# Kernel optimization log

Measured on AMD Instinct MI355X. Metric: run time of the kernel, lower is better.

## Reference

```python
import jax, jax.numpy as jnp
import numpy as np

N = 4096
NEG_SLOPE = 0.2


def _gat_layer(x, src, dst, W, Wb, a, ab):
    # h = Linear(x); e_ij = a([h_i, h_j]) for each edge; dense softmax over dim=1; ELU
    h = x @ W + Wb                               # [N, D]
    D = h.shape[-1]
    e = h[src] @ a[:D] + h[dst] @ a[D:] + ab     # [E] per-edge attention logits
    n = x.shape[0]
    attn = jnp.full((n, n), -jnp.inf, dtype=x.dtype).at[src, dst].set(e)
    attn = jnp.where(attn > 0, attn, NEG_SLOPE * attn)   # leaky_relu (keeps -inf)
    attn = jax.nn.softmax(attn, axis=1)
    return jax.nn.elu(attn @ h)                  # sigma = ELU


def _multihead(x, src, dst, hW, hWb, ha, hab, oW, oWb, oa, oab):
    # concat=False: mean over head outputs, then out GATLayer
    heads = jax.vmap(lambda W, Wb, a, ab: _gat_layer(x, src, dst, W, Wb, a, ab))(hW, hWb, ha, hab)
    xm = heads.mean(axis=0)
    return _gat_layer(xm, src, dst, oW, oWb, oa, oab)


def setup_inputs() -> dict:
    key = jax.random.key(0)
    ks = jax.random.split(key, 20)
    in_dim, hid, out_dim, H, E = 512, 256, 128, 4, 131072
    x = jax.random.normal(ks[0], (N, in_dim), jnp.float32)
    edge_index = jax.random.randint(ks[1], (2, E), 0, N)
    # force self loops so every softmax row has at least one finite entry
    edge_index = edge_index.at[:, :N].set(jnp.broadcast_to(jnp.arange(N), (2, N)))

    def lin(k, shape, fan_in):
        return jax.random.uniform(k, shape, jnp.float32, -1.0, 1.0) / np.sqrt(fan_in).astype(np.float32)

    return {
        "x": x,
        "edge_index": edge_index,
        # layer 0 (MultiHeadGAT in_dim->hid)
        "l0_hW": lin(ks[2], (H, in_dim, hid), in_dim),
        "l0_hWb": lin(ks[3], (H, hid), in_dim),
        "l0_ha": lin(ks[4], (H, 2 * hid), 2 * hid),
        "l0_hab": lin(ks[5], (H,), 2 * hid),
        "l0_oW": lin(ks[6], (hid, hid), hid),
        "l0_oWb": lin(ks[7], (hid,), hid),
        "l0_oa": lin(ks[8], (2 * hid,), 2 * hid),
        "l0_oab": lin(ks[9], (), 2 * hid),
        # layer 1 (MultiHeadGAT hid->hid)
        "l1_hW": lin(ks[10], (H, hid, hid), hid),
        "l1_hWb": lin(ks[11], (H, hid), hid),
        "l1_ha": lin(ks[12], (H, 2 * hid), 2 * hid),
        "l1_hab": lin(ks[13], (H,), 2 * hid),
        "l1_oW": lin(ks[14], (hid, hid), hid),
        "l1_oWb": lin(ks[15], (hid,), hid),
        "l1_oa": lin(ks[16], (2 * hid,), 2 * hid),
        "l1_oab": lin(ks[17], (), 2 * hid),
        # final Linear(hid -> out_dim)
        "lin_W": lin(ks[18], (hid, out_dim), hid),
        "lin_b": lin(ks[19], (out_dim,), hid),
    }


def reference(x, edge_index, l0_hW, l0_hWb, l0_ha, l0_hab, l0_oW, l0_oWb, l0_oa, l0_oab,
              l1_hW, l1_hWb, l1_ha, l1_hab, l1_oW, l1_oWb, l1_oa, l1_oab, lin_W, lin_b):
    src, dst = edge_index[0], edge_index[1]
    lrelu = lambda v: jnp.where(v > 0, v, NEG_SLOPE * v)
    h = lrelu(_multihead(x, src, dst, l0_hW, l0_hWb, l0_ha, l0_hab, l0_oW, l0_oWb, l0_oa, l0_oab))
    h = lrelu(_multihead(h, src, dst, l1_hW, l1_hWb, l1_ha, l1_hab, l1_oW, l1_oWb, l1_oa, l1_oab))
    return h @ lin_W + lin_b  # [N, out_dim], flatten(1) is a no-op for 2D
```

## Files before the change

### kernel.cpp

```cpp
#include <hip/hip_runtime.h>
#include <hip/hip_bf16.h>
#include <math.h>

#define NEG_SLOPE 0.2f

constexpr int D = 256;
constexpr int HEADS = 4;
constexpr int MAXB = 128;

typedef __attribute__((ext_vector_type(8))) short short8;
typedef __attribute__((ext_vector_type(4))) float floatx4;

__device__ inline unsigned short bf16_hi_trunc(float v) {
  return (unsigned short)(__float_as_uint(v) >> 16);
}
__device__ inline float bf16_tof(unsigned short u) {
  return __uint_as_float(((unsigned int)u) << 16);
}
__device__ inline unsigned short bf16_rn(float v) {
  unsigned int b = __float_as_uint(v);
  b += 0x7fffu + ((b >> 16) & 1u);
  return (unsigned short)(b >> 16);
}
__device__ inline void split2(float v, unsigned short& hi, unsigned short& lo) {
  hi = bf16_hi_trunc(v);
  lo = bf16_rn(v - bf16_tof(hi));
}

__global__ void fill_kernel(const int* __restrict__ src, const int* __restrict__ dst,
                            int* __restrict__ cnt, int* __restrict__ colb, int E) {
  int k = blockIdx.x * blockDim.x + threadIdx.x;
  if (k < E) {
    int s = src[k];
    int pos = atomicAdd(&cnt[s], 1);
    if (pos < MAXB) colb[s * MAXB + pos] = dst[k];
  }
}

__global__ __launch_bounds__(128) void dedupe_kernel(const int* __restrict__ cnt,
                                                     int* __restrict__ colb, int Nn) {
  __shared__ int cs[MAXB];
  int i = blockIdx.x;
  int len = cnt[i];
  if (len > MAXB) len = MAXB;
  int tid = threadIdx.x;
  if (tid < len) cs[tid] = colb[i * MAXB + tid];
  __syncthreads();
  if (tid < len) {
    int c = cs[tid];
    bool dup = false;
    for (int s2 = 0; s2 < tid; ++s2)
      if (cs[s2] == c) { dup = true; break; }
    if (dup) colb[i * MAXB + tid] = -1;
  }
}

__global__ __launch_bounds__(256) void prep_kernel(
    int* __restrict__ zeroBase, int zeroN,
    const float* __restrict__ x, unsigned short* __restrict__ xhi, unsigned short* __restrict__ xlo,
    int xN4,
    const float* __restrict__ l0hW, unsigned short* __restrict__ l0hHi, unsigned short* __restrict__ l0hLo,
    const float* __restrict__ l1hW, unsigned short* __restrict__ l1hHi, unsigned short* __restrict__ l1hLo,
    const float* __restrict__ l0oW, unsigned short* __restrict__ l0oHi, unsigned short* __restrict__ l0oLo,
    const float* __restrict__ l1oW, unsigned short* __restrict__ l1oHi, unsigned short* __restrict__ l1oLo,
    const float* __restrict__ linW, unsigned short* __restrict__ linHi, unsigned short* __restrict__ linLo) {
  const int b = blockIdx.x;
  const int t = threadIdx.x;
  if (b < 528) {
    int idx = b * 256 + t;
    if (idx < zeroN) zeroBase[idx] = 0;
    return;
  }
  if (b < 2576) {
    int idx = (b - 528) * 256 + t;
    if (idx < xN4) {
      float4 v = ((const float4*)x)[idx];
      ushort4 h, l;
      split2(v.x, h.x, l.x);
      split2(v.y, h.y, l.y);
      split2(v.z, h.z, l.z);
      split2(v.w, h.w, l.w);
      ((ushort4*)xhi)[idx] = h;
      ((ushort4*)xlo)[idx] = l;
    }
    return;
  }
  __shared__ float tile[32][33];
  const int tr = t >> 5, tc = t & 31;
  if (b < 3088) {
    const int bi = b - 2576;
    const int kb = bi & 15;
    const int nb = (bi >> 4) & 7;
    const int h = bi >> 7;
    const int K = 512, N = 256;
    const int k0 = kb * 32, n0 = nb * 32;
    const float* B = l0hW + (size_t)h * K * N;
#pragma unroll
    for (int i = 0; i < 4; ++i)
      tile[tr + 8 * i][tc] = B[(size_t)(k0 + tr + 8 * i) * N + (n0 + tc)];
    __syncthreads();
    unsigned short* Thi = l0hHi + (size_t)h * N * K;
    unsigned short* Tlo = l0hLo + (size_t)h * N * K;
#pragma unroll
    for (int i = 0; i < 4; ++i) {
      int n = n0 + tr + 8 * i, k = k0 + tc;
      float v = tile[tc][tr + 8 * i];
      unsigned short hi, lo;
      split2(v, hi, lo);
      Thi[(size_t)n * K + k] = hi;
      Tlo[(size_t)n * K + k] = lo;
    }
    return;
  }
  const int bi = b - 3088;
  const int kb = bi & 7;
  const int nb = (bi >> 3) & 7;
  const int z = bi >> 6;
  const int K = 256;
  const int N = (z == 6) ? 128 : 256;
  const int k0 = kb * 32, n0 = nb * 32;
  if (n0 >= N) return;
  const float* B;
  unsigned short *Thi, *Tlo;
  if (z < 4) {
    B = l1hW + (size_t)z * K * 256;
    Thi = l1hHi + (size_t)z * 256 * K;
    Tlo = l1hLo + (size_t)z * 256 * K;
  } else if (z == 4) { B = l0oW; Thi = l0oHi; Tlo = l0oLo; }
  else if (z == 5)   { B = l1oW; Thi = l1oHi; Tlo = l1oLo; }
  else               { B = linW; Thi = linHi; Tlo = linLo; }
#pragma unroll
  for (int i = 0; i < 4; ++i)
    tile[tr + 8 * i][tc] = B[(size_t)(k0 + tr + 8 * i) * N + (n0 + tc)];
  __syncthreads();
#pragma unroll
  for (int i = 0; i < 4; ++i) {
    int n = n0 + tr + 8 * i, k = k0 + tc;
    float v = tile[tc][tr + 8 * i];
    unsigned short hi, lo;
    split2(v, hi, lo);
    Thi[(size_t)n * K + k] = hi;
    Tlo[(size_t)n * K + k] = lo;
  }
}

__global__ __launch_bounds__(256) void gemm_mfma_split(
    const unsigned short* __restrict__ Ahi, const unsigned short* __restrict__ Alo,
    const unsigned short* __restrict__ Bthi, const unsigned short* __restrict__ Btlo,
    const float* __restrict__ bias, float* __restrict__ C, unsigned short* __restrict__ Cb,
    const float* __restrict__ aptr, float* __restrict__ alphaB, float* __restrict__ betaB,
    int M, int N, int K) {
  constexpr int LSTR = 72;
  __shared__ unsigned short sA[2][64 * LSTR];
  __shared__ unsigned short sB[2][64 * LSTR];
  const int tid = threadIdx.x;
  const int bm = blockIdx.x * 64;
  const int gn = blockIdx.y * 64;
  const int head = (gn) / N;
  const int bn = gn - head * N;
  const int Htot = (int)((gridDim.y * 64) / N);

  const int lane = tid & 63;
  const int wv = tid >> 6;
  const int wm = (wv & 1) * 32;
  const int wn = (wv >> 1) * 32;
  const int q = lane >> 4;
  const int l15 = lane & 15;

  floatx4 acc[2][2];
#pragma unroll
  for (int i = 0; i < 2; ++i)
#pragma unroll
    for (int j = 0; j < 2; ++j) acc[i][j] = (floatx4)0.0f;

  for (int k0 = 0; k0 < K; k0 += 64) {
    short8 ra[2][2], rb[2][2];
#pragma unroll
    for (int i = 0; i < 2; ++i) {
      const int c = tid + 256 * i;
      const int row = c >> 3, koff = (c & 7) << 3;
      const size_t boff = (size_t)(gn + row) * K + k0 + koff;
      rb[0][i] = *(const short8*)(Bthi + boff);
      rb[1][i] = *(const short8*)(Btlo + boff);
      const size_t aoff = (size_t)(bm + row) * K + k0 + koff;
      ra[0][i] = *(const short8*)(Ahi + aoff);
      ra[1][i] = *(const short8*)(Alo + aoff);
    }
    __syncthreads();
#pragma unroll
    for (int i = 0; i < 2; ++i) {
      const int c = tid + 256 * i;
      const int row = c >> 3, koff = (c & 7) << 3;
      *(short8*)(&sA[0][row * LSTR + koff]) = ra[0][i];
      *(short8*)(&sA[1][row * LSTR + koff]) = ra[1][i];
      *(short8*)(&sB[0][row * LSTR + koff]) = rb[0][i];
      *(short8*)(&sB[1][row * LSTR + koff]) = rb[1][i];
    }
    __syncthreads();
#pragma unroll
    for (int kc = 0; kc < 2; ++kc) {
      const int ko = kc * 32 + q * 8;
      short8 aH[2], aL[2], bH[2], bL[2];
#pragma unroll
      for (int i = 0; i < 2; ++i) {
        aH[i] = *(const short8*)(&sA[0][(wm + i * 16 + l15) * LSTR + ko]);
        aL[i] = *(const short8*)(&sA[1][(wm + i * 16 + l15) * LSTR + ko]);
        bH[i] = *(const short8*)(&sB[0][(wn + i * 16 + l15) * LSTR + ko]);
        bL[i] = *(const short8*)(&sB[1][(wn + i * 16 + l15) * LSTR + ko]);
      }
#pragma unroll
      for (int i = 0; i < 2; ++i)
#pragma unroll
        for (int j = 0; j < 2; ++j) {
          acc[i][j] = __builtin_amdgcn_mfma_f32_16x16x32_bf16(aH[i], bH[j], acc[i][j], 0, 0, 0);
          acc[i][j] = __builtin_amdgcn_mfma_f32_16x16x32_bf16(aH[i], bL[j], acc[i][j], 0, 0, 0);
          acc[i][j] = __builtin_amdgcn_mfma_f32_16x16x32_bf16(aL[i], bH[j], acc[i][j], 0, 0, 0);
        }
    }
  }
  const size_t rowStride = (size_t)Htot * N;
  const size_t headOff = (size_t)head * N;
  const int colh0 = bn + wn + l15;
  const int colh1 = colh0 + 16;
  const float bv0 = bias[head * N + colh0];
  const float bv1 = bias[head * N + colh1];
  float as0 = 0.f, as1 = 0.f, ad0 = 0.f, ad1 = 0.f;
  if (aptr) {
    as0 = aptr[head * 2 * N + colh0];
    as1 = aptr[head * 2 * N + colh1];
    ad0 = aptr[head * 2 * N + N + colh0];
    ad1 = aptr[head * 2 * N + N + colh1];
  }
#pragma unroll
  for (int i = 0; i < 2; ++i) {
    const int rowb = bm + wm + i * 16 + q * 4;
#pragma unroll
    for (int r = 0; r < 4; ++r) {
      const float o0 = acc[i][0][r] + bv0;
      const float o1 = acc[i][1][r] + bv1;
      if (Cb) {
        Cb[(size_t)(rowb + r) * rowStride + headOff + colh0] = bf16_rn(o0);
        Cb[(size_t)(rowb + r) * rowStride + headOff + colh1] = bf16_rn(o1);
      } else {
        C[(size_t)(rowb + r) * N + colh0] = o0;
        C[(size_t)(rowb + r) * N + colh1] = o1;
      }
      if (aptr) {
        float pa = o0 * as0 + o1 * as1;
        float pb = o0 * ad0 + o1 * ad1;
#pragma unroll
        for (int off = 1; off < 16; off <<= 1) {
          pa += __shfl_xor(pa, off, 64);
          pb += __shfl_xor(pb, off, 64);
        }
        if (l15 == 0) {
          atomicAdd(&alphaB[(size_t)(rowb + r) * Htot + head], pa);
          atomicAdd(&betaB[(size_t)(rowb + r) * Htot + head], pb);
        }
      }
    }
  }
}

__global__ __launch_bounds__(256) void gemm_bias(
    const float* __restrict__ A, const float* __restrict__ B,
    const float* __restrict__ bias, float* __restrict__ C,
    int M, int N, int K) {
  __shared__ float As[16][68];
  __shared__ float Bs[16][68];
  const int tid = threadIdx.x;
  const int bm = blockIdx.x * 64;
  const int gn = blockIdx.y * 64;
  const int head = gn / N;
  const int bn = gn - head * N;
  const float* Bh = B + (size_t)head * K * N;

  const int tx = tid & 15;
  const int ty = tid >> 4;
  const int am = tid >> 2;
  const int ak = (tid & 3) << 2;
  const int bk = tid >> 4;
  const int bn4 = (tid & 15) << 2;

  float acc[4][4] = {};

  for (int k0 = 0; k0 < K; k0 += 16) {
    float4 av = *(const float4*)(A + (size_t)(bm + am) * K + (k0 + ak));
    float4 bv = *(const float4*)(Bh + (size_t)(k0 + bk) * N + (bn + bn4));
    __syncthreads();
    As[ak + 0][am] = av.x;
    As[ak + 1][am] = av.y;
    As[ak + 2][am] = av.z;
    As[ak + 3][am] = av.w;
    *(float4*)(&Bs[bk][bn4]) = bv;
    __syncthreads();
#pragma unroll
    for (int k = 0; k < 16; ++k) {
      float4 aa = *(const float4*)(&As[k][ty << 2]);
      float4 bb = *(const float4*)(&Bs[k][tx << 2]);
      acc[0][0] += aa.x * bb.x; acc[0][1] += aa.x * bb.y; acc[0][2] += aa.x * bb.z; acc[0][3] += aa.x * bb.w;
      acc[1][0] += aa.y * bb.x; acc[1][1] += aa.y * bb.y; acc[1][2] += aa.y * bb.z; acc[1][3] += aa.y * bb.w;
      acc[2][0] += aa.z * bb.x; acc[2][1] += aa.z * bb.y; acc[2][2] += aa.z * bb.z; acc[2][3] += aa.z * bb.w;
      acc[3][0] += aa.w * bb.x; acc[3][1] += aa.w * bb.y; acc[3][2] += aa.w * bb.z; acc[3][3] += aa.w * bb.w;
    }
  }
  float* Ch = C + (size_t)head * M * N;
  const float* bh = bias + (size_t)head * N;
  const int ccol = bn + (tx << 2);
  float4 bias4 = *(const float4*)(bh + ccol);
#pragma unroll
  for (int r = 0; r < 4; ++r) {
    int row = bm + (ty << 2) + r;
    float4 o;
    o.x = acc[r][0] + bias4.x;
    o.y = acc[r][1] + bias4.y;
    o.z = acc[r][2] + bias4.z;
    o.w = acc[r][3] + bias4.w;
    *(float4*)(Ch + (size_t)row * N + ccol) = o;
  }
}

__global__ __launch_bounds__(256) void alphabeta_kernel(
    const float* __restrict__ h, const float* __restrict__ a,
    float* __restrict__ alpha, float* __restrict__ beta, int Nn) {
  __shared__ float reda[4], redb[4];
  const int i = blockIdx.x;
  const int hh = blockIdx.y;
  const int tid = threadIdx.x;
  const int lane = tid & 63, wid = tid >> 6;
  float v = h[((size_t)hh * Nn + i) * D + tid];
  float pa = v * a[hh * 2 * D + tid];
  float pb = v * a[hh * 2 * D + D + tid];
#pragma unroll
  for (int off = 32; off > 0; off >>= 1) {
    pa += __shfl_xor(pa, off, 64);
    pb += __shfl_xor(pb, off, 64);
  }
  if (lane == 0) { reda[wid] = pa; redb[wid] = pb; }
  __syncthreads();
  if (tid == 0) {
    alpha[hh * Nn + i] = reda[0] + reda[1] + reda[2] + reda[3];
    beta[hh * Nn + i] = redb[0] + redb[1] + redb[2] + redb[3];
  }
}

__global__ __launch_bounds__(256) void attn4(
    const unsigned short* __restrict__ hB,
    const float* __restrict__ alpha, const float* __restrict__ beta,
    const float* __restrict__ ab, const int* __restrict__ cnt,
    const int* __restrict__ colb,
    unsigned short* __restrict__ oHi, unsigned short* __restrict__ oLo, int Nn) {
  const int tid = threadIdx.x;
  const int lane = tid & 63;
  const int wv = tid >> 6;
  const int i = blockIdx.x * 4 + wv;

  const unsigned short* hL = hB + (lane << 2);
  const float ai0 = alpha[i * HEADS + 0] + ab[0];
  const float ai1 = alpha[i * HEADS + 1] + ab[1];
  const float ai2 = alpha[i * HEADS + 2] + ab[2];
  const float ai3 = alpha[i * HEADS + 3] + ab[3];
  const int start = i * MAXB;
  int len = cnt[i];
  if (len > MAXB) len = MAXB;

  float m0 = -3.0e38f, m1 = -3.0e38f, m2 = -3.0e38f, m3 = -3.0e38f;
  float s0 = 0.f, s1 = 0.f, s2 = 0.f, s3 = 0.f;
  float4 A0 = make_float4(0.f, 0.f, 0.f, 0.f);
  float4 A1 = make_float4(0.f, 0.f, 0.f, 0.f);
  float4 A2 = make_float4(0.f, 0.f, 0.f, 0.f);
  float4 A3 = make_float4(0.f, 0.f, 0.f, 0.f);

  for (int t0 = 0; t0 < len; t0 += 64) {
    const int t = t0 + lane;
    const int c = (t < len) ? colb[start + t] : -1;
    float e0 = -3.0e38f, e1 = -3.0e38f, e2 = -3.0e38f, e3 = -3.0e38f;
    if (c >= 0) {
      const float4 b4 = *(const float4*)(beta + (size_t)c * HEADS);
      e0 = ai0 + b4.x; e1 = ai1 + b4.y; e2 = ai2 + b4.z; e3 = ai3 + b4.w;
      e0 = e0 > 0.0f ? e0 : NEG_SLOPE * e0;
      e1 = e1 > 0.0f ? e1 : NEG_SLOPE * e1;
      e2 = e2 > 0.0f ? e2 : NEG_SLOPE * e2;
      e3 = e3 > 0.0f ? e3 : NEG_SLOPE * e3;
    }
    float c0 = e0, c1 = e1, c2 = e2, c3 = e3;
#pragma unroll
    for (int off = 32; off > 0; off >>= 1) {
      c0 = fmaxf(c0, __shfl_xor(c0, off, 64));
      c1 = fmaxf(c1, __shfl_xor(c1, off, 64));
      c2 = fmaxf(c2, __shfl_xor(c2, off, 64));
      c3 = fmaxf(c3, __shfl_xor(c3, off, 64));
    }
    const float n0 = fmaxf(m0, c0), n1 = fmaxf(m1, c1);
    const float n2 = fmaxf(m2, c2), n3 = fmaxf(m3, c3);
    const float sc0 = __expf(m0 - n0), sc1 = __expf(m1 - n1);
    const float sc2 = __expf(m2 - n2), sc3 = __expf(m3 - n3);
    float w0 = 0.f, w1 = 0.f, w2 = 0.f, w3 = 0.f;
    if (c >= 0) {
      w0 = __expf(e0 - n0); w1 = __expf(e1 - n1);
      w2 = __expf(e2 - n2); w3 = __expf(e3 - n3);
    }
    float q0 = w0, q1 = w1, q2 = w2, q3 = w3;
#pragma unroll
    for (int off = 32; off > 0; off >>= 1) {
      q0 += __shfl_xor(q0, off, 64);
      q1 += __shfl_xor(q1, off, 64);
      q2 += __shfl_xor(q2, off, 64);
      q3 += __shfl_xor(q3, off, 64);
    }
    s0 = s0 * sc0 + q0; s1 = s1 * sc1 + q1;
    s2 = s2 * sc2 + q2; s3 = s3 * sc3 + q3;
    A0.x *= sc0; A0.y *= sc0; A0.z *= sc0; A0.w *= sc0;
    A1.x *= sc1; A1.y *= sc1; A1.z *= sc1; A1.w *= sc1;
    A2.x *= sc2; A2.y *= sc2; A2.z *= sc2; A2.w *= sc2;
    A3.x *= sc3; A3.y *= sc3; A3.z *= sc3; A3.w *= sc3;
    m0 = n0; m1 = n1; m2 = n2; m3 = n3;

    const int cS = (c >= 0) ? c : 0;
    const int cnt2 = min(64, len - t0);
    int j = 0;
    for (; j + 2 <= cnt2; j += 2) {
      const int ca = __shfl(cS, j);
      const int cb = __shfl(cS, j + 1);
      const float wa0 = __shfl(w0, j),     wa1 = __shfl(w1, j);
      const float wa2 = __shfl(w2, j),     wa3 = __shfl(w3, j);
      const float wb0 = __shfl(w0, j + 1), wb1 = __shfl(w1, j + 1);
      const float wb2 = __shfl(w2, j + 1), wb3 = __shfl(w3, j + 1);
      const unsigned short* pa = hL + (size_t)ca * (HEADS * D);
      const unsigned short* pb = hL + (size_t)cb * (HEADS * D);
      const ushort4 ua0 = *(const ushort4*)(pa);
      const ushort4 ua1 = *(const ushort4*)(pa + D);
      const ushort4 ua2 = *(const ushort4*)(pa + 2 * D);
      const ushort4 ua3 = *(const ushort4*)(pa + 3 * D);
      const ushort4 ub0 = *(const ushort4*)(pb);
      const ushort4 ub1 = *(const ushort4*)(pb + D);
      const ushort4 ub2 = *(const ushort4*)(pb + 2 * D);
      const ushort4 ub3 = *(const ushort4*)(pb + 3 * D);
      A0.x += wa0 * bf16_tof(ua0.x); A0.y += wa0 * bf16_tof(ua0.y);
      A0.z += wa0 * bf16_tof(ua0.z); A0.w += wa0 * bf16_tof(ua0.w);
      A1.x += wa1 * bf16_tof(ua1.x); A1.y += wa1 * bf16_tof(ua1.y);
      A1.z += wa1 * bf16_tof(ua1.z); A1.w += wa1 * bf16_tof(ua1.w);
      A2.x += wa2 * bf16_tof(ua2.x); A2.y += wa2 * bf16_tof(ua2.y);
      A2.z += wa2 * bf16_tof(ua2.z); A2.w += wa2 * bf16_tof(ua2.w);
      A3.x += wa3 * bf16_tof(ua3.x); A3.y += wa3 * bf16_tof(ua3.y);
      A3.z += wa3 * bf16_tof(ua3.z); A3.w += wa3 * bf16_tof(ua3.w);
      A0.x += wb0 * bf16_tof(ub0.x); A0.y += wb0 * bf16_tof(ub0.y);
      A0.z += wb0 * bf16_tof(ub0.z); A0.w += wb0 * bf16_tof(ub0.w);
      A1.x += wb1 * bf16_tof(ub1.x); A1.y += wb1 * bf16_tof(ub1.y);
      A1.z += wb1 * bf16_tof(ub1.z); A1.w += wb1 * bf16_tof(ub1.w);
      A2.x += wb2 * bf16_tof(ub2.x); A2.y += wb2 * bf16_tof(ub2.y);
      A2.z += wb2 * bf16_tof(ub2.z); A2.w += wb2 * bf16_tof(ub2.w);
      A3.x += wb3 * bf16_tof(ub3.x); A3.y += wb3 * bf16_tof(ub3.y);
      A3.z += wb3 * bf16_tof(ub3.z); A3.w += wb3 * bf16_tof(ub3.w);
    }
    for (; j < cnt2; ++j) {
      const int ca = __shfl(cS, j);
      const float wa0 = __shfl(w0, j), wa1 = __shfl(w1, j);
      const float wa2 = __shfl(w2, j), wa3 = __shfl(w3, j);
      const unsigned short* pa = hL + (size_t)ca * (HEADS * D);
      const ushort4 ua0 = *(const ushort4*)(pa);
      const ushort4 ua1 = *(const ushort4*)(pa + D);
      const ushort4 ua2 = *(const ushort4*)(pa + 2 * D);
      const ushort4 ua3 = *(const ushort4*)(pa + 3 * D);
      A0.x += wa0 * bf16_tof(ua0.x); A0.y += wa0 * bf16_tof(ua0.y);
      A0.z += wa0 * bf16_tof(ua0.z); A0.w += wa0 * bf16_tof(ua0.w);
      A1.x += wa1 * bf16_tof(ua1.x); A1.y += wa1 * bf16_tof(ua1.y);
      A1.z += wa1 * bf16_tof(ua1.z); A1.w += wa1 * bf16_tof(ua1.w);
      A2.x += wa2 * bf16_tof(ua2.x); A2.y += wa2 * bf16_tof(ua2.y);
      A2.z += wa2 * bf16_tof(ua2.z); A2.w += wa2 * bf16_tof(ua2.w);
      A3.x += wa3 * bf16_tof(ua3.x); A3.y += wa3 * bf16_tof(ua3.y);
      A3.z += wa3 * bf16_tof(ua3.z); A3.w += wa3 * bf16_tof(ua3.w);
    }
  }

  const float i0 = 1.0f / s0, i1 = 1.0f / s1, i2 = 1.0f / s2, i3 = 1.0f / s3;
  auto elu = [](float x) { return x > 0.0f ? x : expm1f(x); };
  float4 xm;
  xm.x = 0.25f * (elu(A0.x * i0) + elu(A1.x * i1) + elu(A2.x * i2) + elu(A3.x * i3));
  xm.y = 0.25f * (elu(A0.y * i0) + elu(A1.y * i1) + elu(A2.y * i2) + elu(A3.y * i3));
  xm.z = 0.25f * (elu(A0.z * i0) + elu(A1.z * i1) + elu(A2.z * i2) + elu(A3.z * i3));
  xm.w = 0.25f * (elu(A0.w * i0) + elu(A1.w * i1) + elu(A2.w * i2) + elu(A3.w * i3));
  ushort4 h4, l4;
  split2(xm.x, h4.x, l4.x);
  split2(xm.y, h4.y, l4.y);
  split2(xm.z, h4.z, l4.z);
  split2(xm.w, h4.w, l4.w);
  const size_t q4 = ((size_t)i * D >> 2) + lane;
  ((ushort4*)oHi)[q4] = h4;
  ((ushort4*)oLo)[q4] = l4;
}

template <int BF16H>
__global__ __launch_bounds__(256) void attn2(
    const float* __restrict__ h, const unsigned short* __restrict__ hB,
    const float* __restrict__ alpha, const float* __restrict__ beta,
    const float* __restrict__ ab, const int* __restrict__ cnt,
    const int* __restrict__ colb, float* __restrict__ out,
    unsigned short* __restrict__ oHi, unsigned short* __restrict__ oLo,
    int Nn, int H, int mode) {
  const int tid = threadIdx.x;
  const int lane = tid & 63;
  const int wv = tid >> 6;
  const int bx = blockIdx.x;
  const int head = bx % H;
  const int rowblk = bx / H;
  const int i = rowblk * 4 + wv;

  const float* hL = BF16H ? nullptr : (h + (size_t)head * Nn * D + (lane << 2));
  const unsigned short* hLB = BF16H ? (hB + (size_t)head * Nn * D + (lane << 2)) : nullptr;
  const float* betaH = beta + (size_t)head * Nn;
  const float ai = alpha[head * Nn + i] + ab[head];
  const int start = i * MAXB;
  int len = cnt[i];
  if (len > MAXB) len = MAXB;

  float m = -3.0e38f, s = 0.0f;
  float4 acc0 = make_float4(0.0f, 0.0f, 0.0f, 0.0f);
  float4 acc1 = make_float4(0.0f, 0.0f, 0.0f, 0.0f);

  for (int t0 = 0; t0 < len; t0 += 64) {
    const int t = t0 + lane;
    const int c = (t < len) ? colb[start + t] : -1;
    float e = -3.0e38f;
    if (c >= 0) {
      e = ai + betaH[c];
      e = e > 0.0f ? e : NEG_SLOPE * e;
    }
    float cm = e;
#pragma unroll
    for (int off = 32; off > 0; off >>= 1) cm = fmaxf(cm, __shfl_xor(cm, off, 64));
    const float newm = fmaxf(m, cm);
    const float scale = __expf(m - newm);
    const float w = (c >= 0) ? __expf(e - newm) : 0.0f;
    float cs = w;
#pragma unroll
    for (int off = 32; off > 0; off >>= 1) cs += __shfl_xor(cs, off, 64);
    s = s * scale + cs;
    acc0.x *= scale; acc0.y *= scale; acc0.z *= scale; acc0.w *= scale;
    acc1.x *= scale; acc1.y *= scale; acc1.z *= scale; acc1.w *= scale;
    m = newm;

    const int cS = (c >= 0) ? c : 0;
    const int cnt2 = min(64, len - t0);
    int j = 0;
    if constexpr (BF16H) {
      for (; j + 4 <= cnt2; j += 4) {
        const int c0 = __shfl(cS, j);     const float w0 = __shfl(w, j);
        const int c1 = __shfl(cS, j + 1); const float w1 = __shfl(w, j + 1);
        const int c2 = __shfl(cS, j + 2); const float w2 = __shfl(w, j + 2);
        const int c3 = __shfl(cS, j + 3); const float w3 = __shfl(w, j + 3);
        const ushort4 u0 = *(const ushort4*)(hLB + (size_t)c0 * D);
        const ushort4 u1 = *(const ushort4*)(hLB + (size_t)c1 * D);
        const ushort4 u2 = *(const ushort4*)(hLB + (size_t)c2 * D);
        const ushort4 u3 = *(const ushort4*)(hLB + (size_t)c3 * D);
        acc0.x += w0 * bf16_tof(u0.x); acc0.y += w0 * bf16_tof(u0.y);
        acc0.z += w0 * bf16_tof(u0.z); acc0.w += w0 * bf16_tof(u0.w);
        acc1.x += w1 * bf16_tof(u1.x); acc1.y += w1 * bf16_tof(u1.y);
        acc1.z += w1 * bf16_tof(u1.z); acc1.w += w1 * bf16_tof(u1.w);
        acc0.x += w2 * bf16_tof(u2.x); acc0.y += w2 * bf16_tof(u2.y);
        acc0.z += w2 * bf16_tof(u2.z); acc0.w += w2 * bf16_tof(u2.w);
        acc1.x += w3 * bf16_tof(u3.x); acc1.y += w3 * bf16_tof(u3.y);
        acc1.z += w3 * bf16_tof(u3.z); acc1.w += w3 * bf16_tof(u3.w);
      }
      for (; j < cnt2; ++j) {
        const int cj = __shfl(cS, j);
        const float wj = __shfl(w, j);
        const ushort4 u = *(const ushort4*)(hLB + (size_t)cj * D);
        acc0.x += wj * bf16_tof(u.x); acc0.y += wj * bf16_tof(u.y);
        acc0.z += wj * bf16_tof(u.z); acc0.w += wj * bf16_tof(u.w);
      }
    } else {
      for (; j + 4 <= cnt2; j += 4) {
        const int c0 = __shfl(cS, j);     const float w0 = __shfl(w, j);
        const int c1 = __shfl(cS, j + 1); const float w1 = __shfl(w, j + 1);
        const int c2 = __shfl(cS, j + 2); const float w2 = __shfl(w, j + 2);
        const int c3 = __shfl(cS, j + 3); const float w3 = __shfl(w, j + 3);
        const float4 h0 = *(const float4*)(hL + (size_t)c0 * D);
        const float4 h1 = *(const float4*)(hL + (size_t)c1 * D);
        const float4 h2 = *(const float4*)(hL + (size_t)c2 * D);
        const float4 h3 = *(const float4*)(hL + (size_t)c3 * D);
        acc0.x += w0 * h0.x; acc0.y += w0 * h0.y; acc0.z += w0 * h0.z; acc0.w += w0 * h0.w;
        acc1.x += w1 * h1.x; acc1.y += w1 * h1.y; acc1.z += w1 * h1.z; acc1.w += w1 * h1.w;
        acc0.x += w2 * h2.x; acc0.y += w2 * h2.y; acc0.z += w2 * h2.z; acc0.w += w2 * h2.w;
        acc1.x += w3 * h3.x; acc1.y += w3 * h3.y; acc1.z += w3 * h3.z; acc1.w += w3 * h3.w;
      }
      for (; j < cnt2; ++j) {
        const int cj = __shfl(cS, j);
        const float wj = __shfl(w, j);
        const float4 hv = *(const float4*)(hL + (size_t)cj * D);
        acc0.x += wj * hv.x; acc0.y += wj * hv.y;
        acc0.z += wj * hv.z; acc0.w += wj * hv.w;
      }
    }
  }

  const float inv = 1.0f / s;
  float4 v;
  v.x = (acc0.x + acc1.x) * inv; v.y = (acc0.y + acc1.y) * inv;
  v.z = (acc0.z + acc1.z) * inv; v.w = (acc0.w + acc1.w) * inv;
  v.x = v.x > 0.0f ? v.x : expm1f(v.x);
  v.y = v.y > 0.0f ? v.y : expm1f(v.y);
  v.z = v.z > 0.0f ? v.z : expm1f(v.z);
  v.w = v.w > 0.0f ? v.w : expm1f(v.w);

  if (mode == 1 || mode == 3) {
    v.x = v.x > 0.0f ? v.x : NEG_SLOPE * v.x;
    v.y = v.y > 0.0f ? v.y : NEG_SLOPE * v.y;
    v.z = v.z > 0.0f ? v.z : NEG_SLOPE * v.z;
    v.w = v.w > 0.0f ? v.w : NEG_SLOPE * v.w;
    if (mode == 1) {
      *(float4*)(out + (size_t)i * D + (lane << 2)) = v;
    } else {
      ushort4 h4, l4;
      split2(v.x, h4.x, l4.x);
      split2(v.y, h4.y, l4.y);
      split2(v.z, h4.z, l4.z);
      split2(v.w, h4.w, l4.w);
      const size_t q4 = ((size_t)i * D >> 2) + lane;
      ((ushort4*)oHi)[q4] = h4;
      ((ushort4*)oLo)[q4] = l4;
    }
  } else if (mode == 0) {
    if constexpr (BF16H) {
      ushort4 h4;
      h4.x = bf16_rn(v.x);
      h4.y = bf16_rn(v.y);
      h4.z = bf16_rn(v.z);
      h4.w = bf16_rn(v.w);
      const size_t q4 = (((size_t)head * Nn + i) * D >> 2) + lane;
      ((ushort4*)oHi)[q4] = h4;
    } else {
      *(float4*)(out + ((size_t)head * Nn + i) * D + (lane << 2)) = v;
    }
  } else {
    const float invH = 1.0f / (float)H;
    float* o = out + (size_t)i * D + (lane << 2);
    atomicAdd(o + 0, invH * v.x);
    atomicAdd(o + 1, invH * v.y);
    atomicAdd(o + 2, invH * v.z);
    atomicAdd(o + 3, invH * v.w);
  }
}

__global__ __launch_bounds__(256) void mean4_kernel(
    float* __restrict__ hsep, int total4) {
  int idx = blockIdx.x * blockDim.x + threadIdx.x;
  if (idx < total4) {
    float4* p = (float4*)hsep;
    float4 a = p[idx], b = p[idx + total4], c = p[idx + 2 * total4], d = p[idx + 3 * total4];
    float4 o;
    o.x = 0.25f * (a.x + b.x + c.x + d.x);
    o.y = 0.25f * (a.y + b.y + c.y + d.y);
    o.z = 0.25f * (a.z + b.z + c.z + d.z);
    o.w = 0.25f * (a.w + b.w + c.w + d.w);
    p[idx] = o;
  }
}

__global__ void zero_ints(int* __restrict__ p, int n) {
  int i = blockIdx.x * blockDim.x + threadIdx.x;
  if (i < n) p[i] = 0;
}

__global__ void zero_floats(float* __restrict__ p, int n) {
  int i = blockIdx.x * blockDim.x + threadIdx.x;
  if (i < n) p[i] = 0.0f;
}

extern "C" void kernel_launch(void* const* d_in, const int* in_sizes, int n_in,
                              void* d_out, int out_size, void* d_ws, size_t ws_size,
                              hipStream_t stream) {
  const float* x = (const float*)d_in[0];
  const int* eidx = (const int*)d_in[1];
  const float* l0_hW = (const float*)d_in[2];
  const float* l0_hWb = (const float*)d_in[3];
  const float* l0_ha = (const float*)d_in[4];
  const float* l0_hab = (const float*)d_in[5];
  const float* l0_oW = (const float*)d_in[6];
  const float* l0_oWb = (const float*)d_in[7];
  const float* l0_oa = (const float*)d_in[8];
  const float* l0_oab = (const float*)d_in[9];
  const float* l1_hW = (const float*)d_in[10];
  const float* l1_hWb = (const float*)d_in[11];
  const float* l1_ha = (const float*)d_in[12];
  const float* l1_hab = (const float*)d_in[13];
  const float* l1_oW = (const float*)d_in[14];
  const float* l1_oWb = (const float*)d_in[15];
  const float* l1_oa = (const float*)d_in[16];
  const float* l1_oab = (const float*)d_in[17];
  const float* lin_W = (const float*)d_in[18];
  const float* lin_b = (const float*)d_in[19];

  const int in_dim = 512;
  const int Nn = in_sizes[0] / in_dim;
  const int E = in_sizes[1] / 2;
  const int out_dim = 128;

  char* wsp = (char*)d_ws;
  auto alloc = [&](size_t bytes) {
    char* p = wsp;
    wsp += (bytes + 255) & ~(size_t)255;
    return p;
  };
  const size_t ndBytes = sizeof(float) * (size_t)Nn * D;
  const size_t mfmaNeed = 52000000;
  const bool mfma = ws_size >= mfmaNeed;

  if (mfma) {
    unsigned short* hbufB = (unsigned short*)alloc((size_t)HEADS * Nn * D * 2);
    unsigned short* houtB = (unsigned short*)alloc((size_t)Nn * D * 2);
    unsigned short* xmHi  = (unsigned short*)alloc((size_t)Nn * D * 2);
    unsigned short* xmLo  = (unsigned short*)alloc((size_t)Nn * D * 2);
    unsigned short* xhi  = (unsigned short*)alloc((size_t)Nn * in_dim * 2);
    unsigned short* xlo  = (unsigned short*)alloc((size_t)Nn * in_dim * 2);
    unsigned short* x1hi = xhi;
    unsigned short* x1lo = xlo;
    unsigned short* l0hHi = (unsigned short*)alloc((size_t)HEADS * in_dim * D * 2);
    unsigned short* l0hLo = (unsigned short*)alloc((size_t)HEADS * in_dim * D * 2);
    unsigned short* l1hHi = (unsigned short*)alloc((size_t)HEADS * D * D * 2);
    unsigned short* l1hLo = (unsigned short*)alloc((size_t)HEADS * D * D * 2);
    unsigned short* l0oHi = (unsigned short*)alloc((size_t)D * D * 2);
    unsigned short* l0oLo = (unsigned short*)alloc((size_t)D * D * 2);
    unsigned short* l1oHi = (unsigned short*)alloc((size_t)D * D * 2);
    unsigned short* l1oLo = (unsigned short*)alloc((size_t)D * D * 2);
    unsigned short* linHi = (unsigned short*)alloc((size_t)D * out_dim * 2);
    unsigned short* linLo = (unsigned short*)alloc((size_t)D * out_dim * 2);
    int* cnt     = (int*)alloc(sizeof(int) * Nn);
    float* abz   = (float*)alloc(sizeof(float) * 4 * 2 * HEADS * (size_t)Nn);
    int* colb    = (int*)alloc(sizeof(int) * (size_t)Nn * MAXB);
    auto alphaS = [&](int s) { return abz + (size_t)s * 2 * HEADS * Nn; };
    auto betaS  = [&](int s) { return abz + (size_t)s * 2 * HEADS * Nn + HEADS * Nn; };

    const int* src = eidx;
    const int* dst = eidx + E;

    const int zeroN = Nn + 4 * 2 * HEADS * Nn;
    prep_kernel<<<3536, 256, 0, stream>>>(
        cnt, zeroN,
        x, xhi, xlo, Nn * in_dim / 4,
        l0_hW, l0hHi, l0hLo, l1_hW, l1hHi, l1hLo,
        l0_oW, l0oHi, l0oLo, l1_oW, l1oHi, l1oLo, lin_W, linHi, linLo);

    fill_kernel<<<(E + 255) / 256, 256, 0, stream>>>(src, dst, cnt, colb, E);
    dedupe_kernel<<<Nn, 128, 0, stream>>>(cnt, colb, Nn);

    gemm_mfma_split<<<dim3(Nn / 64, HEADS * D / 64), 256, 0, stream>>>(
        xhi, xlo, l0hHi, l0hLo, l0_hWb, nullptr, hbufB,
        l0_ha, alphaS(0), betaS(0), Nn, D, in_dim);
    attn4<<<Nn / 4, 256, 0, stream>>>(hbufB, alphaS(0), betaS(0), l0_hab,
                                      cnt, colb, xmHi, xmLo, Nn);
    gemm_mfma_split<<<dim3(Nn / 64, D / 64), 256, 0, stream>>>(
        xmHi, xmLo, l0oHi, l0oLo, l0_oWb, nullptr, houtB,
        l0_oa, alphaS(1), betaS(1), Nn, D, D);
    attn2<1><<<Nn / 4, 256, 0, stream>>>(nullptr, houtB, alphaS(1), betaS(1), l0_oab,
                                         cnt, colb, nullptr, x1hi, x1lo, Nn, 1, 3);

    gemm_mfma_split<<<dim3(Nn / 64, HEADS * D / 64), 256, 0, stream>>>(
        x1hi, x1lo, l1hHi, l1hLo, l1_hWb, nullptr, hbufB,
        l1_ha, alphaS(2), betaS(2), Nn, D, D);
    attn4<<<Nn / 4, 256, 0, stream>>>(hbufB, alphaS(2), betaS(2), l1_hab,
                                      cnt, colb, xmHi, xmLo, Nn);
    gemm_mfma_split<<<dim3(Nn / 64, D / 64), 256, 0, stream>>>(
        xmHi, xmLo, l1oHi, l1oLo, l1_oWb, nullptr, houtB,
        l1_oa, alphaS(3), betaS(3), Nn, D, D);
    attn2<1><<<Nn / 4, 256, 0, stream>>>(nullptr, houtB, alphaS(3), betaS(3), l1_oab,
                                         cnt, colb, nullptr, x1hi, x1lo, Nn, 1, 3);

    gemm_mfma_split<<<dim3(Nn / 64, out_dim / 64), 256, 0, stream>>>(
        x1hi, x1lo, linHi, linLo, lin_b, (float*)d_out, nullptr,
        nullptr, nullptr, nullptr, Nn, out_dim, D);
    return;
  }

  const size_t smallBytes = sizeof(float) * 2 * HEADS * (size_t)Nn + sizeof(int) * (Nn + (size_t)Nn * MAXB) + 4096;
  const bool staged = ws_size >= (8 * ndBytes + 2 * ndBytes + smallBytes + 65536);

  float* hbuf  = (float*)alloc(ndBytes * HEADS);
  float* hsep  = staged ? (float*)alloc(ndBytes * HEADS) : nullptr;
  float* xm    = staged ? hsep : (float*)alloc(ndBytes);
  float* x1    = (float*)alloc(ndBytes);
  float* hout  = (float*)alloc(ndBytes);
  float* alpha = (float*)alloc(sizeof(float) * HEADS * (size_t)Nn);
  float* beta  = (float*)alloc(sizeof(float) * HEADS * (size_t)Nn);
  int* cnt     = (int*)alloc(sizeof(int) * Nn);
  int* colb    = (int*)alloc(sizeof(int) * (size_t)Nn * MAXB);

  const int* src = eidx;
  const int* dst = eidx + E;

  zero_ints<<<(Nn + 255) / 256, 256, 0, stream>>>(cnt, Nn);
  fill_kernel<<<(E + 255) / 256, 256, 0, stream>>>(src, dst, cnt, colb, E);
  dedupe_kernel<<<Nn, 128, 0, stream>>>(cnt, colb, Nn);

  const int total4 = Nn * D / 4;
  const int meanBlocks = (total4 + 255) / 256;

  gemm_bias<<<dim3(Nn / 64, HEADS * D / 64), 256, 0, stream>>>(x, l0_hW, l0_hWb, hbuf, Nn, D, in_dim);
  alphabeta_kernel<<<dim3(Nn, HEADS), 256, 0, stream>>>(hbuf, l0_ha, alpha, beta, Nn);
  if (staged) {
    attn2<0><<<HEADS * (Nn / 4), 256, 0, stream>>>(hbuf, nullptr, alpha, beta, l0_hab, cnt, colb, hsep, nullptr, nullptr, Nn, HEADS, 0);
    mean4_kernel<<<meanBlocks, 256, 0, stream>>>(hsep, total4);
  } else {
    zero_floats<<<(Nn * D + 255) / 256, 256, 0, stream>>>(xm, Nn * D);
    attn2<0><<<HEADS * (Nn / 4), 256, 0, stream>>>(hbuf, nullptr, alpha, beta, l0_hab, cnt, colb, xm, nullptr, nullptr, Nn, HEADS, 2);
  }
  gemm_bias<<<dim3(Nn / 64, D / 64), 256, 0, stream>>>(xm, l0_oW, l0_oWb, hout, Nn, D, D);
  alphabeta_kernel<<<dim3(Nn, 1), 256, 0, stream>>>(hout, l0_oa, alpha, beta, Nn);
  attn2<0><<<Nn / 4, 256, 0, stream>>>(hout, nullptr, alpha, beta, l0_oab, cnt, colb, x1, nullptr, nullptr, Nn, 1, 1);

  gemm_bias<<<dim3(Nn / 64, HEADS * D / 64), 256, 0, stream>>>(x1, l1_hW, l1_hWb, hbuf, Nn, D, D);
  alphabeta_kernel<<<dim3(Nn, HEADS), 256, 0, stream>>>(hbuf, l1_ha, alpha, beta, Nn);
  if (staged) {
    attn2<0><<<HEADS * (Nn / 4), 256, 0, stream>>>(hbuf, nullptr, alpha, beta, l1_hab, cnt, colb, hsep, nullptr, nullptr, Nn, HEADS, 0);
    mean4_kernel<<<meanBlocks, 256, 0, stream>>>(hsep, total4);
  } else {
    zero_floats<<<(Nn * D + 255) / 256, 256, 0, stream>>>(xm, Nn * D);
    attn2<0><<<HEADS * (Nn / 4), 256, 0, stream>>>(hbuf, nullptr, alpha, beta, l1_hab, cnt, colb, xm, nullptr, nullptr, Nn, HEADS, 2);
  }
  gemm_bias<<<dim3(Nn / 64, D / 64), 256, 0, stream>>>(xm, l1_oW, l1_oWb, hout, Nn, D, D);
  alphabeta_kernel<<<dim3(Nn, 1), 256, 0, stream>>>(hout, l1_oa, alpha, beta, Nn);
  attn2<0><<<Nn / 4, 256, 0, stream>>>(hout, nullptr, alpha, beta, l1_oab, cnt, colb, x1, nullptr, nullptr, Nn, 1, 1);

  gemm_bias<<<dim3(Nn / 64, out_dim / 64), 256, 0, stream>>>(x1, lin_W, lin_b, (float*)d_out, Nn, out_dim, D);
}
```

Measured before the change: 272.7 us.

## Use direct global-to-LDS loads with XOR swizzle and staged vectorized bf16 stores

The split-bf16 MFMA GEMM now loads its tiles with global_load_lds, so the data goes straight from global memory into LDS without passing through registers. Each wave loads one plane (A hi/lo or B hi/lo), and the row padding is replaced by an XOR swizzle to avoid bank conflicts. The bf16 output is first staged in LDS and then written with coalesced 16-byte vector stores instead of scattered 2-byte stores. The cost is extra barriers, and the loads are still not double-buffered.

Measured after the change: 276.9 us. Within noise of the previous version (+1.6%).

```diff
diff --git a/kernel.cpp b/kernel.cpp
--- a/kernel.cpp
+++ b/kernel.cpp
@@ -25,6 +25,12 @@
 __device__ inline void split2(float v, unsigned short& hi, unsigned short& lo) {
   hi = bf16_hi_trunc(v);
   lo = bf16_rn(v - bf16_tof(hi));
+}
+
+__device__ inline void gld_lds16(const unsigned short* gsrc, unsigned short* ldst) {
+  __builtin_amdgcn_global_load_lds(
+      (const __attribute__((address_space(1))) unsigned int*)gsrc,
+      (__attribute__((address_space(3))) unsigned int*)ldst, 16, 0, 0);
 }
 
 __global__ void fill_kernel(const int* __restrict__ src, const int* __restrict__ dst,
@@ -150,13 +156,12 @@
     const float* __restrict__ bias, float* __restrict__ C, unsigned short* __restrict__ Cb,
     const float* __restrict__ aptr, float* __restrict__ alphaB, float* __restrict__ betaB,
     int M, int N, int K) {
-  constexpr int LSTR = 72;
-  __shared__ unsigned short sA[2][64 * LSTR];
-  __shared__ unsigned short sB[2][64 * LSTR];
+  __shared__ unsigned short sA[2][64 * 64];
+  __shared__ unsigned short sB[2][64 * 64];
   const int tid = threadIdx.x;
   const int bm = blockIdx.x * 64;
   const int gn = blockIdx.y * 64;
-  const int head = (gn) / N;
+  const int head = gn / N;
   const int bn = gn - head * N;
   const int Htot = (int)((gridDim.y * 64) / N);
 
@@ -167,6 +172,12 @@
   const int q = lane >> 4;
   const int l15 = lane & 15;
 
+  unsigned short* myPlane = (wv == 0) ? &sA[0][0] : (wv == 1) ? &sA[1][0]
+                          : (wv == 2) ? &sB[0][0] : &sB[1][0];
+  const unsigned short* mySrc = (wv == 0) ? Ahi : (wv == 1) ? Alo
+                              : (wv == 2) ? Bthi : Btlo;
+  const int myBase = (wv < 2) ? bm : gn;
+
   floatx4 acc[2][2];
 #pragma unroll
   for (int i = 0; i < 2; ++i)
@@ -174,39 +185,29 @@
     for (int j = 0; j < 2; ++j) acc[i][j] = (floatx4)0.0f;
 
   for (int k0 = 0; k0 < K; k0 += 64) {
-    short8 ra[2][2], rb[2][2];
-#pragma unroll
-    for (int i = 0; i < 2; ++i) {
-      const int c = tid + 256 * i;
-      const int row = c >> 3, koff = (c & 7) << 3;
-      const size_t boff = (size_t)(gn + row) * K + k0 + koff;
-      rb[0][i] = *(const short8*)(Bthi + boff);
-      rb[1][i] = *(const short8*)(Btlo + boff);
-      const size_t aoff = (size_t)(bm + row) * K + k0 + koff;
-      ra[0][i] = *(const short8*)(Ahi + aoff);
-      ra[1][i] = *(const short8*)(Alo + aoff);
+    if (k0 != 0) __syncthreads();
+#pragma unroll
+    for (int i = 0; i < 8; ++i) {
+      const int c = i * 64 + lane;
+      const int row = c >> 3;
+      const int col = (c & 7) ^ (row & 7);
+      gld_lds16(mySrc + (size_t)(myBase + row) * K + k0 + col * 8,
+                myPlane + i * 512);
     }
     __syncthreads();
 #pragma unroll
-    for (int i = 0; i < 2; ++i) {
-      const int c = tid + 256 * i;
-      const int row = c >> 3, koff = (c & 7) << 3;
-      *(short8*)(&sA[0][row * LSTR + koff]) = ra[0][i];
-      *(short8*)(&sA[1][row * LSTR + koff]) = ra[1][i];
-      *(short8*)(&sB[0][row * LSTR + koff]) = rb[0][i];
-      *(short8*)(&sB[1][row * LSTR + koff]) = rb[1][i];
-    }
-    __syncthreads();
-#pragma unroll
     for (int kc = 0; kc < 2; ++kc) {
-      const int ko = kc * 32 + q * 8;
       short8 aH[2], aL[2], bH[2], bL[2];
 #pragma unroll
       for (int i = 0; i < 2; ++i) {
-        aH[i] = *(const short8*)(&sA[0][(wm + i * 16 + l15) * LSTR + ko]);
-        aL[i] = *(const short8*)(&sA[1][(wm + i * 16 + l15) * LSTR + ko]);
-        bH[i] = *(const short8*)(&sB[0][(wn + i * 16 + l15) * LSTR + ko]);
-        bL[i] = *(const short8*)(&sB[1][(wn + i * 16 + l15) * LSTR + ko]);
+        const int ra = wm + i * 16 + l15;
+        const int rb = wn + i * 16 + l15;
+        const int xa = (kc * 4 + q) ^ (ra & 7);
+        const int xb = (kc * 4 + q) ^ (rb & 7);
+        aH[i] = *(const short8*)(&sA[0][ra * 64 + xa * 8]);
+        aL[i] = *(const short8*)(&sA[1][ra * 64 + xa * 8]);
+        bH[i] = *(const short8*)(&sB[0][rb * 64 + xb * 8]);
+        bL[i] = *(const short8*)(&sB[1][rb * 64 + xb * 8]);
       }
 #pragma unroll
       for (int i = 0; i < 2; ++i)
@@ -218,6 +219,7 @@
         }
     }
   }
+
   const size_t rowStride = (size_t)Htot * N;
   const size_t headOff = (size_t)head * N;
   const int colh0 = bn + wn + l15;
@@ -231,19 +233,21 @@
     ad0 = aptr[head * 2 * N + N + colh0];
     ad1 = aptr[head * 2 * N + N + colh1];
   }
+  __syncthreads();
+  unsigned short* sOut = &sA[0][0];
 #pragma unroll
   for (int i = 0; i < 2; ++i) {
-    const int rowb = bm + wm + i * 16 + q * 4;
+    const int rloc = wm + i * 16 + q * 4;
 #pragma unroll
     for (int r = 0; r < 4; ++r) {
       const float o0 = acc[i][0][r] + bv0;
       const float o1 = acc[i][1][r] + bv1;
       if (Cb) {
-        Cb[(size_t)(rowb + r) * rowStride + headOff + colh0] = bf16_rn(o0);
-        Cb[(size_t)(rowb + r) * rowStride + headOff + colh1] = bf16_rn(o1);
+        sOut[(rloc + r) * 72 + wn + l15] = bf16_rn(o0);
+        sOut[(rloc + r) * 72 + wn + 16 + l15] = bf16_rn(o1);
       } else {
-        C[(size_t)(rowb + r) * N + colh0] = o0;
-        C[(size_t)(rowb + r) * N + colh1] = o1;
+        C[(size_t)(bm + rloc + r) * N + colh0] = o0;
+        C[(size_t)(bm + rloc + r) * N + colh1] = o1;
       }
       if (aptr) {
         float pa = o0 * as0 + o1 * as1;
@@ -254,10 +258,21 @@
           pb += __shfl_xor(pb, off, 64);
         }
         if (l15 == 0) {
-          atomicAdd(&alphaB[(size_t)(rowb + r) * Htot + head], pa);
-          atomicAdd(&betaB[(size_t)(rowb + r) * Htot + head], pb);
+          atomicAdd(&alphaB[(size_t)(bm + rloc + r) * Htot + head], pa);
+          atomicAdd(&betaB[(size_t)(bm + rloc + r) * Htot + head], pb);
         }
       }
+    }
+  }
+  if (Cb) {
+    __syncthreads();
+#pragma unroll
+    for (int e = 0; e < 2; ++e) {
+      const int flat = tid + 256 * e;
+      const int row = flat >> 3;
+      const int col = (flat & 7) * 8;
+      short8 v = *(const short8*)(&sOut[row * 72 + col]);
+      *(short8*)(Cb + (size_t)(bm + row) * rowStride + headOff + bn + col) = v;
     }
   }
 }
```
